# Kernel optimization log

Measured on AMD Instinct MI355X. Metric: run time of the kernel, lower is better.

## Reference

```python
import jax, jax.numpy as jnp
import numpy as np

N = 500_000          # num nodes
K = 3                # neighbors per star subgraph = graphlet_size - 1
E = N * K            # one subgraph per node -> directed (center, nbr) edges
L = 2                # hop_neighbor
FD = 2               # final_dim = 2**pqc_dim
H = 64               # hidden_dim
NC = 8               # num_classes
NIN = 16             # node_input_dim
EIN = 8              # edge_input_dim


def _lin(k, i, o):
    # torch.nn.Linear-style init scale
    return jax.random.normal(k, (i, o), jnp.float32) * (1.0 / np.sqrt(i))


def setup_inputs() -> dict:
    key = jax.random.key(0)
    ks = jax.random.split(key, 32)
    node_feat = jax.random.normal(ks[0], (N, NIN), jnp.float32)
    edge_attr = jax.random.normal(ks[1], (E, EIN), jnp.float32)
    # edge e = (center, neighbor); centers grouped: edges 3i..3i+2 belong to node i
    centers = jnp.repeat(jnp.arange(N, dtype=jnp.int32), K)
    neighbors = jax.random.randint(ks[2], (E,), 0, N, dtype=jnp.int32)
    edge_index = jnp.stack([centers, neighbors])  # [2, E]
    batch = jnp.zeros((N,), jnp.int32)
    msg_W1 = jnp.stack([_lin(ks[6 + i], 2 * FD, H) for i in range(L)])
    msg_W2 = jnp.stack([_lin(ks[8 + i], H, FD) for i in range(L)])
    upd_W1 = jnp.stack([_lin(ks[10 + i], 2 * FD, H) for i in range(L)])
    upd_W2 = jnp.stack([_lin(ks[12 + i], H, FD) for i in range(L)])
    return dict(
        node_feat=node_feat, edge_attr=edge_attr, edge_index=edge_index, batch=batch,
        Wn=_lin(ks[3], NIN, FD), bn=jnp.zeros((FD,), jnp.float32),
        We=_lin(ks[4], EIN, FD), be=jnp.zeros((FD,), jnp.float32),
        msg_W1=msg_W1, msg_b1=jnp.zeros((L, H), jnp.float32),
        msg_W2=msg_W2, msg_b2=jnp.zeros((L, FD), jnp.float32),
        upd_W1=upd_W1, upd_b1=jnp.zeros((L, H), jnp.float32),
        upd_W2=upd_W2, upd_b2=jnp.zeros((L, FD), jnp.float32),
        fin_W1=_lin(ks[14], FD, H), fin_b1=jnp.zeros((H,), jnp.float32),
        fin_W2=_lin(ks[15], H, NC), fin_b2=jnp.zeros((NC,), jnp.float32),
    )


def _leaky(x):
    return jnp.where(x >= 0, x, 0.1 * x)


def _mlp(x, W1, b1, W2, b2):
    # MLP([din, 64, dout], act=LeakyReLU(0.1)); dropout inactive at eval
    return _leaky(x @ W1 + b1) @ W2 + b2


def reference(node_feat, edge_attr, edge_index, batch, Wn, bn, We, be,
              msg_W1, msg_b1, msg_W2, msg_b2, upd_W1, upd_b1, upd_W2, upd_b2,
              fin_W1, fin_b1, fin_W2, fin_b2):
    ctr = edge_index[0]  # [E] center of each star edge
    nbr = edge_index[1]  # [E] neighbor
    h = node_feat @ Wn + bn      # [N, FD] input_node projection
    e = edge_attr @ We + be      # [E, FD] input_edge projection (fixed across layers)
    for l in range(L):
        # message over each (center, neighbor) edge: concat(edge_feat, nbr_feat)
        msg = _mlp(jnp.concatenate([e, h[nbr]], axis=1),
                   msg_W1[l], msg_b1[l], msg_W2[l], msg_b2[l])  # [E, FD]
        aggr = jax.ops.segment_sum(msg, ctr, num_segments=N)    # [N, FD]
        new = _mlp(jnp.concatenate([h, aggr], axis=1),
                   upd_W1[l], upd_b1[l], upd_W2[l], upd_b2[l])  # [N, FD]
        h = jax.nn.relu(h + new)  # updates_node[center] += new_center; then ReLU
    return _mlp(h, fin_W1, fin_b1, fin_W2, fin_b2)  # [N, NC]
```

## Files before the change

### kernel.cpp

```cpp
#include <hip/hip_runtime.h>

#define NN 500000
#define KK 3
#define EE (NN * KK)
#define FD 2
#define HH 64
#define NC 8
#define NIN 16
#define EIN 8

__device__ __forceinline__ float leaky(float x) { return x >= 0.0f ? x : 0.1f * x; }

__global__ __launch_bounds__(256) void prep_kernel(
    const float* __restrict__ node_feat, const float* __restrict__ edge_attr,
    const float* __restrict__ Wn, const float* __restrict__ bn,
    const float* __restrict__ We, const float* __restrict__ be,
    float* __restrict__ h, float* __restrict__ e)
{
    int idx = blockIdx.x * blockDim.x + threadIdx.x;
    if (idx < NN) {
        const float4* x4 = (const float4*)(node_feat + (size_t)idx * NIN);
        float4 v0 = x4[0], v1 = x4[1], v2 = x4[2], v3 = x4[3];
        float xs[16] = {v0.x, v0.y, v0.z, v0.w, v1.x, v1.y, v1.z, v1.w,
                        v2.x, v2.y, v2.z, v2.w, v3.x, v3.y, v3.z, v3.w};
        float a0 = bn[0], a1 = bn[1];
#pragma unroll
        for (int i = 0; i < NIN; i++) {
            a0 = fmaf(xs[i], Wn[i * FD + 0], a0);
            a1 = fmaf(xs[i], Wn[i * FD + 1], a1);
        }
        ((float2*)h)[idx] = make_float2(a0, a1);
    } else if (idx < NN + EE) {
        int eidx = idx - NN;
        const float4* x4 = (const float4*)(edge_attr + (size_t)eidx * EIN);
        float4 v0 = x4[0], v1 = x4[1];
        float xs[8] = {v0.x, v0.y, v0.z, v0.w, v1.x, v1.y, v1.z, v1.w};
        float a0 = be[0], a1 = be[1];
#pragma unroll
        for (int i = 0; i < EIN; i++) {
            a0 = fmaf(xs[i], We[i * FD + 0], a0);
            a1 = fmaf(xs[i], We[i * FD + 1], a1);
        }
        ((float2*)e)[eidx] = make_float2(a0, a1);
    }
}

__global__ __launch_bounds__(256) void layer_kernel(
    const float* __restrict__ h_in, const float* __restrict__ e,
    const int* __restrict__ nbr,
    const float* __restrict__ mW1g, const float* __restrict__ mb1g,
    const float* __restrict__ mW2g, const float* __restrict__ mb2g,
    const float* __restrict__ uW1g, const float* __restrict__ ub1g,
    const float* __restrict__ uW2g, const float* __restrict__ ub2g,
    float* __restrict__ h_out,
    const float* __restrict__ fW1g, const float* __restrict__ fb1g,
    const float* __restrict__ fW2g, const float* __restrict__ fb2g,
    float* __restrict__ out)
{
    __shared__ float sW1[4 * HH], sb1[HH], sW2[2 * HH], sb2[2];
    __shared__ float uW1[4 * HH], ub1[HH], uW2[2 * HH], ub2[2];
    __shared__ float fW1[2 * HH], fb1[HH], fW2[HH * NC], fb2[NC];
    int t = threadIdx.x;
    sW1[t] = mW1g[t];
    uW1[t] = uW1g[t];
    if (t < HH) { sb1[t] = mb1g[t]; ub1[t] = ub1g[t]; }
    if (t < 2 * HH) { sW2[t] = mW2g[t]; uW2[t] = uW2g[t]; }
    if (t < 2) { sb2[t] = mb2g[t]; ub2[t] = ub2g[t]; }
    if (out) {
        if (t < 2 * HH) fW1[t] = fW1g[t];
        if (t < HH) fb1[t] = fb1g[t];
        if (t < NC) fb2[t] = fb2g[t];
        fW2[t] = fW2g[t];
        fW2[t + 256] = fW2g[t + 256];
    }
    __syncthreads();

    int i = blockIdx.x * blockDim.x + t;
    if (i >= NN) return;

    float2 hh = ((const float2*)h_in)[i];
    int base = i * KK;
    int n0 = nbr[base + 0], n1 = nbr[base + 1], n2 = nbr[base + 2];
    float2 hn0 = ((const float2*)h_in)[n0];
    float2 hn1 = ((const float2*)h_in)[n1];
    float2 hn2 = ((const float2*)h_in)[n2];
    float2 e0 = ((const float2*)e)[base + 0];
    float2 e1 = ((const float2*)e)[base + 1];
    float2 e2 = ((const float2*)e)[base + 2];

    float a0 = 3.0f * sb2[0], a1 = 3.0f * sb2[1];
#pragma unroll 8
    for (int j = 0; j < HH; j++) {
        float w0 = sW1[j], w1 = sW1[HH + j], w2 = sW1[2 * HH + j], w3 = sW1[3 * HH + j];
        float bb = sb1[j];
        float t0 = fmaf(e0.x, w0, fmaf(e0.y, w1, fmaf(hn0.x, w2, fmaf(hn0.y, w3, bb))));
        float t1 = fmaf(e1.x, w0, fmaf(e1.y, w1, fmaf(hn1.x, w2, fmaf(hn1.y, w3, bb))));
        float t2 = fmaf(e2.x, w0, fmaf(e2.y, w1, fmaf(hn2.x, w2, fmaf(hn2.y, w3, bb))));
        float ts = leaky(t0) + leaky(t1) + leaky(t2);
        a0 = fmaf(ts, sW2[2 * j + 0], a0);
        a1 = fmaf(ts, sW2[2 * j + 1], a1);
    }

    float u0 = ub2[0], u1 = ub2[1];
#pragma unroll 8
    for (int j = 0; j < HH; j++) {
        float tt = fmaf(hh.x, uW1[j],
                   fmaf(hh.y, uW1[HH + j],
                   fmaf(a0, uW1[2 * HH + j],
                   fmaf(a1, uW1[3 * HH + j], ub1[j]))));
        tt = leaky(tt);
        u0 = fmaf(tt, uW2[2 * j + 0], u0);
        u1 = fmaf(tt, uW2[2 * j + 1], u1);
    }
    float nh0 = fmaxf(hh.x + u0, 0.0f);
    float nh1 = fmaxf(hh.y + u1, 0.0f);

    if (!out) {
        ((float2*)h_out)[i] = make_float2(nh0, nh1);
    } else {
        float o[NC];
#pragma unroll
        for (int c = 0; c < NC; c++) o[c] = fb2[c];
#pragma unroll 4
        for (int j = 0; j < HH; j++) {
            float tt = leaky(fmaf(nh0, fW1[j], fmaf(nh1, fW1[HH + j], fb1[j])));
#pragma unroll
            for (int c = 0; c < NC; c++) o[c] = fmaf(tt, fW2[j * NC + c], o[c]);
        }
        float4* op = (float4*)(out + (size_t)i * NC);
        op[0] = make_float4(o[0], o[1], o[2], o[3]);
        op[1] = make_float4(o[4], o[5], o[6], o[7]);
    }
}

extern "C" void kernel_launch(void* const* d_in, const int* in_sizes, int n_in,
                              void* d_out, int out_size, void* d_ws, size_t ws_size,
                              hipStream_t stream) {
    const float* node_feat = (const float*)d_in[0];
    const float* edge_attr = (const float*)d_in[1];
    const int* edge_index = (const int*)d_in[2];
    const float* Wn = (const float*)d_in[4];
    const float* bn = (const float*)d_in[5];
    const float* We = (const float*)d_in[6];
    const float* be = (const float*)d_in[7];
    const float* msgW1 = (const float*)d_in[8];
    const float* msgb1 = (const float*)d_in[9];
    const float* msgW2 = (const float*)d_in[10];
    const float* msgb2 = (const float*)d_in[11];
    const float* updW1 = (const float*)d_in[12];
    const float* updb1 = (const float*)d_in[13];
    const float* updW2 = (const float*)d_in[14];
    const float* updb2 = (const float*)d_in[15];
    const float* finW1 = (const float*)d_in[16];
    const float* finb1 = (const float*)d_in[17];
    const float* finW2 = (const float*)d_in[18];
    const float* finb2 = (const float*)d_in[19];
    float* out = (float*)d_out;

    const int* nbr = edge_index + EE;

    char* ws = (char*)d_ws;
    float* hA = (float*)ws;
    float* hB = (float*)(ws + (size_t)NN * 2 * 4);
    float* eP = (float*)(ws + (size_t)NN * 4 * 4);

    const int threads = 256;
    int prep_grid = (NN + EE + threads - 1) / threads;
    prep_kernel<<<prep_grid, threads, 0, stream>>>(node_feat, edge_attr, Wn, bn, We, be, hA, eP);

    int grid = (NN + threads - 1) / threads;
    layer_kernel<<<grid, threads, 0, stream>>>(
        hA, eP, nbr,
        msgW1, msgb1, msgW2, msgb2,
        updW1, updb1, updW2, updb2,
        hB, nullptr, nullptr, nullptr, nullptr, nullptr);
    layer_kernel<<<grid, threads, 0, stream>>>(
        hB, eP, nbr,
        msgW1 + 4 * HH, msgb1 + HH, msgW2 + 2 * HH, msgb2 + FD,
        updW1 + 4 * HH, updb1 + HH, updW2 + 2 * HH, updb2 + FD,
        nullptr, finW1, finb1, finW2, finb2, out);
}
```

Baseline: 227.3 us.

## Load MLP weights via scalar loads into SGPRs instead of shared memory

Replaces the per-block LDS staging of MLP weights (with __syncthreads) by inline-asm s_load_dwordx* scalar loads that keep the uniform weights in SGPRs, so FMAs take scalar operands directly. The inner loops are chunked by 8 hidden units, each chunk issuing scalar loads followed by an explicit lgkmcnt wait. The FINAL flag becomes a template parameter and leaky is rewritten as fmaxf. This removes LDS traffic and block barriers but serializes the scalar-load latency per chunk and adds SGPR pressure, and it relies on hand-written asm waits for correctness.

```diff
diff --git a/kernel.cpp b/kernel.cpp
--- a/kernel.cpp
+++ b/kernel.cpp
@@ -3,31 +3,65 @@
 #define NN 500000
 #define KK 3
 #define EE (NN * KK)
-#define FD 2
 #define HH 64
 #define NC 8
 #define NIN 16
 #define EIN 8
 
-__device__ __forceinline__ float leaky(float x) { return x >= 0.0f ? x : 0.1f * x; }
+typedef __attribute__((ext_vector_type(2)))  float sf2;
+typedef __attribute__((ext_vector_type(4)))  float sf4;
+typedef __attribute__((ext_vector_type(8)))  float sf8;
+typedef __attribute__((ext_vector_type(16))) float sf16;
+
+__device__ __forceinline__ sf2 sload2(const float* p) {
+    sf2 r; asm("s_load_dwordx2 %0, %1, 0x0" : "=s"(r) : "s"(p)); return r;
+}
+__device__ __forceinline__ sf4 sload4(const float* p) {
+    sf4 r; asm("s_load_dwordx4 %0, %1, 0x0" : "=s"(r) : "s"(p)); return r;
+}
+__device__ __forceinline__ sf8 sload8(const float* p) {
+    sf8 r; asm("s_load_dwordx8 %0, %1, 0x0" : "=s"(r) : "s"(p)); return r;
+}
+__device__ __forceinline__ sf16 sload16(const float* p) {
+    sf16 r; asm("s_load_dwordx16 %0, %1, 0x0" : "=s"(r) : "s"(p)); return r;
+}
+
+#define SWAIT1(a)           asm volatile("s_waitcnt lgkmcnt(0)" : "+s"(a))
+#define SWAIT2(a,b)         asm volatile("s_waitcnt lgkmcnt(0)" : "+s"(a),"+s"(b))
+#define SWAIT5(a,b,c,d,e)   asm volatile("s_waitcnt lgkmcnt(0)" : "+s"(a),"+s"(b),"+s"(c),"+s"(d),"+s"(e))
+#define SWAIT6(a,b,c,d,e,f) asm volatile("s_waitcnt lgkmcnt(0)" : "+s"(a),"+s"(b),"+s"(c),"+s"(d),"+s"(e),"+s"(f))
+
+__device__ __forceinline__ float leaky(float x) { return fmaxf(x, 0.1f * x); }
 
 __global__ __launch_bounds__(256) void prep_kernel(
     const float* __restrict__ node_feat, const float* __restrict__ edge_attr,
     const float* __restrict__ Wn, const float* __restrict__ bn,
     const float* __restrict__ We, const float* __restrict__ be,
-    float* __restrict__ h, float* __restrict__ e)
+    float* __restrict__ h, float* __restrict__ ep)
 {
-    int idx = blockIdx.x * blockDim.x + threadIdx.x;
+    sf16 wn0 = sload16(Wn);
+    sf16 wn1 = sload16(Wn + 16);
+    sf2  bnv = sload2(bn);
+    sf16 wev = sload16(We);
+    sf2  bev = sload2(be);
+    SWAIT5(wn0, wn1, bnv, wev, bev);
+
+    int idx = blockIdx.x * 256 + threadIdx.x;
     if (idx < NN) {
         const float4* x4 = (const float4*)(node_feat + (size_t)idx * NIN);
         float4 v0 = x4[0], v1 = x4[1], v2 = x4[2], v3 = x4[3];
         float xs[16] = {v0.x, v0.y, v0.z, v0.w, v1.x, v1.y, v1.z, v1.w,
                         v2.x, v2.y, v2.z, v2.w, v3.x, v3.y, v3.z, v3.w};
-        float a0 = bn[0], a1 = bn[1];
-#pragma unroll
-        for (int i = 0; i < NIN; i++) {
-            a0 = fmaf(xs[i], Wn[i * FD + 0], a0);
-            a1 = fmaf(xs[i], Wn[i * FD + 1], a1);
+        float a0 = bnv.x, a1 = bnv.y;
+#pragma unroll
+        for (int i = 0; i < 8; i++) {
+            a0 = fmaf(xs[i], wn0[2 * i], a0);
+            a1 = fmaf(xs[i], wn0[2 * i + 1], a1);
+        }
+#pragma unroll
+        for (int i = 0; i < 8; i++) {
+            a0 = fmaf(xs[8 + i], wn1[2 * i], a0);
+            a1 = fmaf(xs[8 + i], wn1[2 * i + 1], a1);
         }
         ((float2*)h)[idx] = make_float2(a0, a1);
     } else if (idx < NN + EE) {
@@ -35,48 +69,35 @@
         const float4* x4 = (const float4*)(edge_attr + (size_t)eidx * EIN);
         float4 v0 = x4[0], v1 = x4[1];
         float xs[8] = {v0.x, v0.y, v0.z, v0.w, v1.x, v1.y, v1.z, v1.w};
-        float a0 = be[0], a1 = be[1];
-#pragma unroll
-        for (int i = 0; i < EIN; i++) {
-            a0 = fmaf(xs[i], We[i * FD + 0], a0);
-            a1 = fmaf(xs[i], We[i * FD + 1], a1);
-        }
-        ((float2*)e)[eidx] = make_float2(a0, a1);
-    }
-}
-
+        float a0 = bev.x, a1 = bev.y;
+#pragma unroll
+        for (int i = 0; i < 8; i++) {
+            a0 = fmaf(xs[i], wev[2 * i], a0);
+            a1 = fmaf(xs[i], wev[2 * i + 1], a1);
+        }
+        ((float2*)ep)[eidx] = make_float2(a0, a1);
+    }
+}
+
+template<bool FINAL>
 __global__ __launch_bounds__(256) void layer_kernel(
     const float* __restrict__ h_in, const float* __restrict__ e,
     const int* __restrict__ nbr,
-    const float* __restrict__ mW1g, const float* __restrict__ mb1g,
-    const float* __restrict__ mW2g, const float* __restrict__ mb2g,
-    const float* __restrict__ uW1g, const float* __restrict__ ub1g,
-    const float* __restrict__ uW2g, const float* __restrict__ ub2g,
+    const float* __restrict__ mW1, const float* __restrict__ mb1,
+    const float* __restrict__ mW2, const float* __restrict__ mb2,
+    const float* __restrict__ uW1, const float* __restrict__ ub1,
+    const float* __restrict__ uW2, const float* __restrict__ ub2,
     float* __restrict__ h_out,
-    const float* __restrict__ fW1g, const float* __restrict__ fb1g,
-    const float* __restrict__ fW2g, const float* __restrict__ fb2g,
+    const float* __restrict__ fW1, const float* __restrict__ fb1,
+    const float* __restrict__ fW2, const float* __restrict__ fb2,
     float* __restrict__ out)
 {
-    __shared__ float sW1[4 * HH], sb1[HH], sW2[2 * HH], sb2[2];
-    __shared__ float uW1[4 * HH], ub1[HH], uW2[2 * HH], ub2[2];
-    __shared__ float fW1[2 * HH], fb1[HH], fW2[HH * NC], fb2[NC];
-    int t = threadIdx.x;
-    sW1[t] = mW1g[t];
-    uW1[t] = uW1g[t];
-    if (t < HH) { sb1[t] = mb1g[t]; ub1[t] = ub1g[t]; }
-    if (t < 2 * HH) { sW2[t] = mW2g[t]; uW2[t] = uW2g[t]; }
-    if (t < 2) { sb2[t] = mb2g[t]; ub2[t] = ub2g[t]; }
-    if (out) {
-        if (t < 2 * HH) fW1[t] = fW1g[t];
-        if (t < HH) fb1[t] = fb1g[t];
-        if (t < NC) fb2[t] = fb2g[t];
-        fW2[t] = fW2g[t];
-        fW2[t + 256] = fW2g[t + 256];
-    }
-    __syncthreads();
-
-    int i = blockIdx.x * blockDim.x + t;
+    int i = blockIdx.x * 256 + threadIdx.x;
     if (i >= NN) return;
+
+    sf2 mb2v = sload2(mb2);
+    sf2 ub2v = sload2(ub2);
+    SWAIT2(mb2v, ub2v);
 
     float2 hh = ((const float2*)h_in)[i];
     int base = i * KK;
@@ -88,44 +109,73 @@
     float2 e1 = ((const float2*)e)[base + 1];
     float2 e2 = ((const float2*)e)[base + 2];
 
-    float a0 = 3.0f * sb2[0], a1 = 3.0f * sb2[1];
-#pragma unroll 8
-    for (int j = 0; j < HH; j++) {
-        float w0 = sW1[j], w1 = sW1[HH + j], w2 = sW1[2 * HH + j], w3 = sW1[3 * HH + j];
-        float bb = sb1[j];
-        float t0 = fmaf(e0.x, w0, fmaf(e0.y, w1, fmaf(hn0.x, w2, fmaf(hn0.y, w3, bb))));
-        float t1 = fmaf(e1.x, w0, fmaf(e1.y, w1, fmaf(hn1.x, w2, fmaf(hn1.y, w3, bb))));
-        float t2 = fmaf(e2.x, w0, fmaf(e2.y, w1, fmaf(hn2.x, w2, fmaf(hn2.y, w3, bb))));
-        float ts = leaky(t0) + leaky(t1) + leaky(t2);
-        a0 = fmaf(ts, sW2[2 * j + 0], a0);
-        a1 = fmaf(ts, sW2[2 * j + 1], a1);
-    }
-
-    float u0 = ub2[0], u1 = ub2[1];
-#pragma unroll 8
-    for (int j = 0; j < HH; j++) {
-        float tt = fmaf(hh.x, uW1[j],
-                   fmaf(hh.y, uW1[HH + j],
-                   fmaf(a0, uW1[2 * HH + j],
-                   fmaf(a1, uW1[3 * HH + j], ub1[j]))));
-        tt = leaky(tt);
-        u0 = fmaf(tt, uW2[2 * j + 0], u0);
-        u1 = fmaf(tt, uW2[2 * j + 1], u1);
+    float a0 = 3.0f * mb2v.x, a1 = 3.0f * mb2v.y;
+#pragma unroll 1
+    for (int j0 = 0; j0 < HH; j0 += 8) {
+        sf8 w0 = sload8(mW1 + j0);
+        sf8 w1 = sload8(mW1 + HH + j0);
+        sf8 w2 = sload8(mW1 + 2 * HH + j0);
+        sf8 w3 = sload8(mW1 + 3 * HH + j0);
+        sf8 bb = sload8(mb1 + j0);
+        sf16 wc = sload16(mW2 + 2 * j0);
+        SWAIT6(w0, w1, w2, w3, bb, wc);
+#pragma unroll
+        for (int q = 0; q < 8; q++) {
+            float t0 = fmaf(e0.x, w0[q], fmaf(e0.y, w1[q], fmaf(hn0.x, w2[q], fmaf(hn0.y, w3[q], bb[q]))));
+            float t1 = fmaf(e1.x, w0[q], fmaf(e1.y, w1[q], fmaf(hn1.x, w2[q], fmaf(hn1.y, w3[q], bb[q]))));
+            float t2 = fmaf(e2.x, w0[q], fmaf(e2.y, w1[q], fmaf(hn2.x, w2[q], fmaf(hn2.y, w3[q], bb[q]))));
+            float ts = leaky(t0) + leaky(t1) + leaky(t2);
+            a0 = fmaf(ts, wc[2 * q], a0);
+            a1 = fmaf(ts, wc[2 * q + 1], a1);
+        }
+    }
+
+    float u0 = ub2v.x, u1 = ub2v.y;
+#pragma unroll 1
+    for (int j0 = 0; j0 < HH; j0 += 8) {
+        sf8 w0 = sload8(uW1 + j0);
+        sf8 w1 = sload8(uW1 + HH + j0);
+        sf8 w2 = sload8(uW1 + 2 * HH + j0);
+        sf8 w3 = sload8(uW1 + 3 * HH + j0);
+        sf8 bb = sload8(ub1 + j0);
+        sf16 wc = sload16(uW2 + 2 * j0);
+        SWAIT6(w0, w1, w2, w3, bb, wc);
+#pragma unroll
+        for (int q = 0; q < 8; q++) {
+            float tt = fmaf(hh.x, w0[q], fmaf(hh.y, w1[q], fmaf(a0, w2[q], fmaf(a1, w3[q], bb[q]))));
+            tt = leaky(tt);
+            u0 = fmaf(tt, wc[2 * q], u0);
+            u1 = fmaf(tt, wc[2 * q + 1], u1);
+        }
     }
     float nh0 = fmaxf(hh.x + u0, 0.0f);
     float nh1 = fmaxf(hh.y + u1, 0.0f);
 
-    if (!out) {
+    if (!FINAL) {
         ((float2*)h_out)[i] = make_float2(nh0, nh1);
     } else {
+        sf8 fb2v = sload8(fb2);
+        SWAIT1(fb2v);
         float o[NC];
 #pragma unroll
-        for (int c = 0; c < NC; c++) o[c] = fb2[c];
-#pragma unroll 4
-        for (int j = 0; j < HH; j++) {
-            float tt = leaky(fmaf(nh0, fW1[j], fmaf(nh1, fW1[HH + j], fb1[j])));
-#pragma unroll
-            for (int c = 0; c < NC; c++) o[c] = fmaf(tt, fW2[j * NC + c], o[c]);
+        for (int c = 0; c < NC; c++) o[c] = fb2v[c];
+#pragma unroll 1
+        for (int j0 = 0; j0 < HH; j0 += 4) {
+            sf4 p0 = sload4(fW1 + j0);
+            sf4 p1 = sload4(fW1 + HH + j0);
+            sf4 pb = sload4(fb1 + j0);
+            sf16 q0 = sload16(fW2 + 8 * j0);
+            sf16 q1 = sload16(fW2 + 8 * j0 + 16);
+            SWAIT5(p0, p1, pb, q0, q1);
+#pragma unroll
+            for (int qq = 0; qq < 4; qq++) {
+                float tt = leaky(fmaf(nh0, p0[qq], fmaf(nh1, p1[qq], pb[qq])));
+#pragma unroll
+                for (int c = 0; c < NC; c++) {
+                    float wv = (qq < 2) ? q0[8 * qq + c] : q1[8 * (qq - 2) + c];
+                    o[c] = fmaf(tt, wv, o[c]);
+                }
+            }
         }
         float4* op = (float4*)(out + (size_t)i * NC);
         op[0] = make_float4(o[0], o[1], o[2], o[3]);
@@ -169,14 +219,14 @@
     prep_kernel<<<prep_grid, threads, 0, stream>>>(node_feat, edge_attr, Wn, bn, We, be, hA, eP);
 
     int grid = (NN + threads - 1) / threads;
-    layer_kernel<<<grid, threads, 0, stream>>>(
+    layer_kernel<false><<<grid, threads, 0, stream>>>(
         hA, eP, nbr,
         msgW1, msgb1, msgW2, msgb2,
         updW1, updb1, updW2, updb2,
-        hB, nullptr, nullptr, nullptr, nullptr, nullptr);
-    layer_kernel<<<grid, threads, 0, stream>>>(
+        hB, finW1, finb1, finW2, finb2, nullptr);
+    layer_kernel<true><<<grid, threads, 0, stream>>>(
         hB, eP, nbr,
-        msgW1 + 4 * HH, msgb1 + HH, msgW2 + 2 * HH, msgb2 + FD,
-        updW1 + 4 * HH, updb1 + HH, updW2 + 2 * HH, updb2 + FD,
+        msgW1 + 4 * HH, msgb1 + HH, msgW2 + 2 * HH, msgb2 + 2,
+        updW1 + 4 * HH, updb1 + HH, updW2 + 2 * HH, updb2 + 2,
         nullptr, finW1, finb1, finW2, finb2, out);
 }
```

Result: faster. 213.9 us (-5.9%).
